# Performance work log

Measured on AMD Instinct MI355X. Metric: run time of the kernel, lower is better.

The kernel has to match this reference:

```python
import jax, jax.numpy as jnp
import numpy as np
import math

B, N, D = 2, 4096, 1024
NUM_LAYERS = 12
INIT_RANGE = 0.02


def setup_inputs() -> dict:
    key = jax.random.key(0)
    k1, k2 = jax.random.split(key)
    hidden_states = jax.random.normal(k1, (B, N, D), dtype=jnp.float32)
    std = INIT_RANGE / math.sqrt(2.0 * NUM_LAYERS * D)
    queries = jax.random.normal(k2, (D, D), dtype=jnp.float32) * std
    return {"hidden_states": hidden_states, "queries": queries}


def reference(hidden_states, queries):
    # Q = F.linear(X, W) = X @ W^T  -> [B, N, D]
    q = jnp.einsum('bnd,ed->bne', hidden_states, queries)
    # pre_attn = Q @ X^T  -> [B, N, N]
    pre_attn = jnp.einsum('bne,bme->bnm', q, hidden_states)
    # attention = pre_attn @ X  -> [B, N, D]
    attention = jnp.einsum('bnm,bmd->bnd', pre_attn, hidden_states)
    return attention
```

## Files before the change

### kernel.cpp

```cpp
#include <hip/hip_runtime.h>
#include <hip/hip_bf16.h>
#include <stdint.h>

using bf16 = __hip_bfloat16;
typedef __attribute__((ext_vector_type(8))) short short8;
typedef __attribute__((ext_vector_type(4))) float f32x4;

#define BM 128
#define BK 32

__device__ __forceinline__ void g2lds16(const void* g, void* l) {
    __builtin_amdgcn_global_load_lds(
        (const __attribute__((address_space(1))) void*)g,
        (__attribute__((address_space(3))) void*)l,
        16, 0, 0);
}

__device__ __forceinline__ short f2bs(float x) {
    union { bf16 h; short s; } u;
    u.h = __float2bfloat16(x);
    return u.s;
}

__device__ __forceinline__ int bswz(int row, int cg) { return cg ^ ((row >> 1) & 3); }
__device__ __forceinline__ int fswz(int row, int cg) { return cg ^ (row & 7); }

__global__ __launch_bounds__(256)
void transpose_cvt(const float* __restrict__ src, ushort* __restrict__ dstT,
                   ushort* __restrict__ dstN,
                   int R, int C, long sstride, long dstrideT, long dstrideN)
{
    __shared__ __align__(16) ushort t[64][72];
    const float* s = src + (size_t)blockIdx.z * sstride;
    ushort*      dT = dstT + (size_t)blockIdx.z * dstrideT;
    const int r0 = blockIdx.y * 64, c0 = blockIdx.x * 64;
    const int tid = threadIdx.x;
#pragma unroll
    for (int ii = 0; ii < 4; ++ii) {
        int idx = ii * 256 + tid;
        int r = idx >> 4, c4 = (idx & 15) * 4;
        float4 v = *(const float4*)&s[(size_t)(r0 + r) * C + c0 + c4];
        union { ushort u[4]; uint2 q; } o;
        o.u[0] = (ushort)f2bs(v.x); o.u[1] = (ushort)f2bs(v.y);
        o.u[2] = (ushort)f2bs(v.z); o.u[3] = (ushort)f2bs(v.w);
        *(uint2*)&t[r][c4] = o.q;
        if (dstN) {
            ushort* dN = dstN + (size_t)blockIdx.z * dstrideN;
            *(uint2*)&dN[(size_t)(r0 + r) * C + c0 + c4] = o.q;
        }
    }
    __syncthreads();
#pragma unroll
    for (int ii = 0; ii < 2; ++ii) {
        int idx = ii * 256 + tid;
        int c = idx >> 3, r8 = (idx & 7) * 8;
        union { ushort u[8]; uint4 v; } tmp;
#pragma unroll
        for (int j = 0; j < 8; ++j) tmp.u[j] = t[r8 + j][c];
        *(uint4*)&dT[(size_t)(c0 + c) * R + r0 + r8] = tmp.v;
    }
}

template <int MODE, int A_F32, int NFRAG>
__global__ __launch_bounds__(256)
void gemm_bt(const void* __restrict__ Av, const bf16* __restrict__ B,
             void* __restrict__ Cv, int M, int N, int K, int kChunks,
             long sA, long sB, long sC)
{
    constexpr int BN  = 32 * NFRAG;
    constexpr int BSH = BN / 64;
    constexpr int ANE = BM * BK * (A_F32 ? 2 : 1);
    __shared__ __align__(16) bf16 lA[2][ANE];
    __shared__ __align__(16) bf16 lB[2][BN * BK];

    const int z     = blockIdx.z;
    const int batch = z / kChunks;
    const int chunk = z - batch * kChunks;
    const int kLen  = K / kChunks;
    const int k0    = chunk * kLen;

    const int gx  = gridDim.x;
    int flat = blockIdx.y * gx + blockIdx.x;
    const int cpx = (gx * gridDim.y) >> 3;
    flat = (flat & 7) * cpx + (flat >> 3);
    const int m0 = (flat / gx) * BM;
    const int n0 = (flat - (flat / gx) * gx) * BN;

    const int tid  = threadIdx.x;
    const int lane = tid & 63;
    const int wave = tid >> 6;
    const int wr   = wave >> 1, wc = wave & 1;
    const int ml   = lane & 15;
    const int q    = lane >> 4;

    const bf16* Bb = B + (size_t)batch * sB;
    const bf16* bp[BSH];
#pragma unroll
    for (int s = 0; s < BSH; ++s) {
        int idx = s * 256 + tid;
        int row = idx >> 2, cg = idx & 3;
        bp[s] = Bb + (size_t)(n0 + row) * K + k0 + 8 * bswz(row, cg);
    }

    const float* a32[4];
    const bf16*  a16[2];
    if constexpr (A_F32) {
        const float* Ab = (const float*)Av + (size_t)batch * sA;
#pragma unroll
        for (int s = 0; s < 4; ++s) {
            int idx = s * 256 + tid;
            int row = idx >> 3, cg = idx & 7;
            a32[s] = Ab + (size_t)(m0 + row) * K + k0 + 4 * fswz(row, cg);
        }
    } else {
        const bf16* Ab = (const bf16*)Av + (size_t)batch * sA;
#pragma unroll
        for (int s = 0; s < 2; ++s) {
            int idx = s * 256 + tid;
            int row = idx >> 2, cg = idx & 3;
            a16[s] = Ab + (size_t)(m0 + row) * K + k0 + 8 * bswz(row, cg);
        }
    }

    f32x4 acc[4][NFRAG] = {};

    auto stage = [&](int buf) {
        if constexpr (A_F32) {
            float* lAf = (float*)lA[buf];
#pragma unroll
            for (int s = 0; s < 4; ++s) {
                g2lds16(a32[s], &lAf[(s * 256 + tid) * 4]);
                a32[s] += BK;
            }
        } else {
#pragma unroll
            for (int s = 0; s < 2; ++s) {
                g2lds16(a16[s], &lA[buf][(s * 256 + tid) * 8]);
                a16[s] += BK;
            }
        }
#pragma unroll
        for (int s = 0; s < BSH; ++s) {
            g2lds16(bp[s], &lB[buf][(s * 256 + tid) * 8]);
            bp[s] += BK;
        }
    };

    auto compute = [&](int buf) {
        const bf16* cA = lA[buf];
        const bf16* cB = lB[buf];
        short8 af[4], bfr[NFRAG];
#pragma unroll
        for (int i = 0; i < 4; ++i) {
            const int rA = wr * 64 + i * 16 + ml;
            if constexpr (A_F32) {
                const float* lAf = (const float*)cA;
                float4 x0 = *(const float4*)&lAf[rA * 32 + 4 * fswz(rA, 2 * q)];
                float4 x1 = *(const float4*)&lAf[rA * 32 + 4 * fswz(rA, 2 * q + 1)];
                af[i][0] = f2bs(x0.x); af[i][1] = f2bs(x0.y);
                af[i][2] = f2bs(x0.z); af[i][3] = f2bs(x0.w);
                af[i][4] = f2bs(x1.x); af[i][5] = f2bs(x1.y);
                af[i][6] = f2bs(x1.z); af[i][7] = f2bs(x1.w);
            } else {
                af[i] = *(const short8*)&cA[rA * 32 + 8 * bswz(rA, q)];
            }
        }
#pragma unroll
        for (int j = 0; j < NFRAG; ++j) {
            const int rB = wc * (16 * NFRAG) + j * 16 + ml;
            bfr[j] = *(const short8*)&cB[rB * 32 + 8 * bswz(rB, q)];
        }
#pragma unroll
        for (int mi = 0; mi < 4; ++mi)
#pragma unroll
            for (int nj = 0; nj < NFRAG; ++nj)
                acc[mi][nj] = __builtin_amdgcn_mfma_f32_16x16x32_bf16(
                    af[mi], bfr[nj], acc[mi][nj], 0, 0, 0);
    };

    const int nk = kLen / BK;
    stage(0);
    __syncthreads();
    int cur = 0;
    for (int kt = 0; kt < nk - 1; ++kt) {
        stage(cur ^ 1);
        compute(cur);
        __syncthreads();
        cur ^= 1;
    }
    compute(cur);

#pragma unroll
    for (int mi = 0; mi < 4; ++mi)
#pragma unroll
        for (int nj = 0; nj < NFRAG; ++nj)
#pragma unroll
            for (int r = 0; r < 4; ++r) {
                int row = m0 + wr * 64 + mi * 16 + q * 4 + r;
                int col = n0 + wc * (16 * NFRAG) + nj * 16 + ml;
                if constexpr (MODE == 1) {
                    float* Cf = (float*)Cv + (size_t)batch * sC;
                    atomicAdd(&Cf[(size_t)row * N + col], acc[mi][nj][r]);
                } else if constexpr (MODE == 0) {
                    ushort* Cb = (ushort*)Cv + (size_t)batch * sC;
                    Cb[(size_t)row * N + col] = (ushort)f2bs(acc[mi][nj][r]);
                } else {
                    float* Cf = (float*)Cv + (size_t)batch * sC;
                    Cf[(size_t)row * N + col] = acc[mi][nj][r];
                }
            }
}

extern "C" void kernel_launch(void* const* d_in, const int* in_sizes, int n_in,
                              void* d_out, int out_size, void* d_ws, size_t ws_size,
                              hipStream_t stream)
{
    const int B = 2, N = 4096, D = 1024;
    const float* X = (const float*)d_in[0];
    const float* W = (const float*)d_in[1];
    float* out = (float*)d_out;

    char* ob = (char*)d_out;
    char* ws = (char*)d_ws;
    ushort* Xt = (ushort*)ob;
    float*  Gf = (float*)(ob + (16ll << 20));
    ushort* Wt = (ushort*)(ob + (28ll << 20));

    const bool bigws = ws_size >= (20ull << 20);
    ushort* Xb = bigws ? (ushort*)ws : nullptr;
    ushort* Mt = (ushort*)(ws + (bigws ? (16ll << 20) : 0));

    transpose_cvt<<<dim3(D / 64, N / 64, B), 256, 0, stream>>>(
        X, Xt, Xb, N, D, (long)N * D, (long)D * N, (long)N * D);
    transpose_cvt<<<dim3(D / 64, D / 64, 1), 256, 0, stream>>>(
        W, Wt, nullptr, D, D, 0, 0, 0);
    (void)hipMemsetAsync(Gf, 0, (size_t)B * D * D * sizeof(float), stream);
    gemm_bt<1, 0, 4><<<dim3(D / 128, D / BM, B * 4), 256, 0, stream>>>(
        (const void*)Xt, (const bf16*)Xt, Gf, D, D, N, 4,
        (long)D * N, (long)D * N, (long)D * D);
    gemm_bt<0, 1, 2><<<dim3(D / 64, D / BM, B), 256, 0, stream>>>(
        (const void*)Gf, (const bf16*)Wt, Mt, D, D, D, 1,
        (long)D * D, 0, (long)D * D);
    if (bigws) {
        gemm_bt<2, 0, 4><<<dim3(D / 128, N / BM, B), 256, 0, stream>>>(
            (const void*)Xb, (const bf16*)Mt, out, N, D, D, 1,
            (long)N * D, (long)D * D, (long)N * D);
    } else {
        gemm_bt<2, 1, 4><<<dim3(D / 128, N / BM, B), 256, 0, stream>>>(
            (const void*)X, (const bf16*)Mt, out, N, D, D, 1,
            (long)N * D, (long)D * D, (long)N * D);
    }
}
```

Measured before the change: 203.1 us.

## Triple-buffer GEMM LDS stages with explicit vmcnt waits and MFMA priority

Replaces the double-buffered K loop with a three-stage LDS ring that prefetches two tiles ahead. Explicit s_waitcnt vmcnt counts and raw s_barrier calls replace __syncthreads. The next stage is issued right after the fragments are read into registers, before the MFMAs. MFMA blocks run at raised wave priority (s_setprio). The aim is to hide global-to-LDS latency and cut barrier stalls, at the cost of 50% more shared memory, which may lower occupancy, and fragile hand-counted wait values.

Result: faster. 182.6 us (-10.1%).

```diff
diff --git a/kernel.cpp b/kernel.cpp
--- a/kernel.cpp
+++ b/kernel.cpp
@@ -14,6 +14,15 @@
         (const __attribute__((address_space(1))) void*)g,
         (__attribute__((address_space(3))) void*)l,
         16, 0, 0);
+}
+
+template <int N>
+__device__ __forceinline__ void s_wait_vmcnt() {
+    asm volatile("s_waitcnt vmcnt(%0)" :: "n"(N) : "memory");
+}
+__device__ __forceinline__ void s_wait_lgkm0() {
+    asm volatile("s_waitcnt lgkmcnt(0)" ::: "memory");
+    __builtin_amdgcn_sched_barrier(0);
 }
 
 __device__ __forceinline__ short f2bs(float x) {
@@ -69,9 +78,11 @@
 {
     constexpr int BN  = 32 * NFRAG;
     constexpr int BSH = BN / 64;
+    constexpr int ASH = A_F32 ? 4 : 2;
+    constexpr int L   = ASH + BSH;
     constexpr int ANE = BM * BK * (A_F32 ? 2 : 1);
-    __shared__ __align__(16) bf16 lA[2][ANE];
-    __shared__ __align__(16) bf16 lB[2][BN * BK];
+    __shared__ __align__(16) bf16 lA[3][ANE];
+    __shared__ __align__(16) bf16 lB[3][BN * BK];
 
     const int z     = blockIdx.z;
     const int batch = z / kChunks;
@@ -146,7 +157,7 @@
         }
     };
 
-    auto compute = [&](int buf) {
+    auto step = [&](int buf, bool doStage) {
         const bf16* cA = lA[buf];
         const bf16* cB = lB[buf];
         short8 af[4], bfr[NFRAG];
@@ -170,25 +181,35 @@
             const int rB = wc * (16 * NFRAG) + j * 16 + ml;
             bfr[j] = *(const short8*)&cB[rB * 32 + 8 * bswz(rB, q)];
         }
+        s_wait_lgkm0();
+        __builtin_amdgcn_s_barrier();
+        if (doStage) stage(buf);
+        __builtin_amdgcn_s_setprio(1);
 #pragma unroll
         for (int mi = 0; mi < 4; ++mi)
 #pragma unroll
             for (int nj = 0; nj < NFRAG; ++nj)
                 acc[mi][nj] = __builtin_amdgcn_mfma_f32_16x16x32_bf16(
                     af[mi], bfr[nj], acc[mi][nj], 0, 0, 0);
+        __builtin_amdgcn_s_setprio(0);
     };
 
     const int nk = kLen / BK;
-    stage(0);
-    __syncthreads();
+    stage(0); stage(1); stage(2);
     int cur = 0;
-    for (int kt = 0; kt < nk - 1; ++kt) {
-        stage(cur ^ 1);
-        compute(cur);
-        __syncthreads();
-        cur ^= 1;
-    }
-    compute(cur);
+    for (int kt = 0; kt < nk - 2; ++kt) {
+        s_wait_vmcnt<2 * L>();
+        __builtin_amdgcn_s_barrier();
+        step(cur, kt < nk - 3);
+        cur = (cur == 2) ? 0 : cur + 1;
+    }
+    s_wait_vmcnt<L>();
+    __builtin_amdgcn_s_barrier();
+    step(cur, false);
+    cur = (cur == 2) ? 0 : cur + 1;
+    s_wait_vmcnt<0>();
+    __builtin_amdgcn_s_barrier();
+    step(cur, false);
 
 #pragma unroll
     for (int mi = 0; mi < 4; ++mi)
```

## Deepen GEMM LDS pipeline to four buffers with explicit vmcnt waits

Applied to the files above, without the earlier changes.

Replaces the double-buffered global-to-LDS staging with a four-stage ring of statically selected LDS buffers. Three tiles are prefetched ahead, and each step waits only on the oldest outstanding loads using s_waitcnt vmcnt instead of a full __syncthreads. This is meant to hide global load latency better and to cut barrier stalls. In exchange it doubles LDS use, which can lower occupancy, and it assumes nk is a multiple of 4 and at least 4.

Measured after the change: 174.7 us. 1.16x faster.

```diff
diff --git a/kernel.cpp b/kernel.cpp
--- a/kernel.cpp
+++ b/kernel.cpp
@@ -8,12 +8,19 @@
 
 #define BM 128
 #define BK 32
+
+template <int V> struct ic { static constexpr int v = V; };
 
 __device__ __forceinline__ void g2lds16(const void* g, void* l) {
     __builtin_amdgcn_global_load_lds(
         (const __attribute__((address_space(1))) void*)g,
         (__attribute__((address_space(3))) void*)l,
         16, 0, 0);
+}
+
+template <int N>
+__device__ __forceinline__ void s_wait_vmcnt() {
+    asm volatile("s_waitcnt vmcnt(%0)" :: "n"(N) : "memory");
 }
 
 __device__ __forceinline__ short f2bs(float x) {
@@ -69,9 +76,12 @@
 {
     constexpr int BN  = 32 * NFRAG;
     constexpr int BSH = BN / 64;
+    constexpr int ASH = A_F32 ? 4 : 2;
+    constexpr int L   = ASH + BSH;
     constexpr int ANE = BM * BK * (A_F32 ? 2 : 1);
-    __shared__ __align__(16) bf16 lA[2][ANE];
-    __shared__ __align__(16) bf16 lB[2][BN * BK];
+    constexpr int BNE = BN * BK;
+    __shared__ __align__(16) bf16 lA0[ANE], lA1[ANE], lA2[ANE], lA3[ANE];
+    __shared__ __align__(16) bf16 lB0[BNE], lB1[BNE], lB2[BNE], lB3[BNE];
 
     const int z     = blockIdx.z;
     const int batch = z / kChunks;
@@ -124,9 +134,26 @@
 
     f32x4 acc[4][NFRAG] = {};
 
-    auto stage = [&](int buf) {
+    auto pickA = [&](auto C) -> bf16* {
+        constexpr int b_ = decltype(C)::v;
+        if constexpr (b_ == 0) return lA0;
+        else if constexpr (b_ == 1) return lA1;
+        else if constexpr (b_ == 2) return lA2;
+        else return lA3;
+    };
+    auto pickB = [&](auto C) -> bf16* {
+        constexpr int b_ = decltype(C)::v;
+        if constexpr (b_ == 0) return lB0;
+        else if constexpr (b_ == 1) return lB1;
+        else if constexpr (b_ == 2) return lB2;
+        else return lB3;
+    };
+
+    auto stage = [&](auto C) {
+        bf16* A_ = pickA(C);
+        bf16* B_ = pickB(C);
         if constexpr (A_F32) {
-            float* lAf = (float*)lA[buf];
+            float* lAf = (float*)A_;
 #pragma unroll
             for (int s = 0; s < 4; ++s) {
                 g2lds16(a32[s], &lAf[(s * 256 + tid) * 4]);
@@ -135,21 +162,20 @@
         } else {
 #pragma unroll
             for (int s = 0; s < 2; ++s) {
-                g2lds16(a16[s], &lA[buf][(s * 256 + tid) * 8]);
+                g2lds16(a16[s], &A_[(s * 256 + tid) * 8]);
                 a16[s] += BK;
             }
         }
 #pragma unroll
         for (int s = 0; s < BSH; ++s) {
-            g2lds16(bp[s], &lB[buf][(s * 256 + tid) * 8]);
+            g2lds16(bp[s], &B_[(s * 256 + tid) * 8]);
             bp[s] += BK;
         }
     };
 
-    auto compute = [&](int buf) {
-        const bf16* cA = lA[buf];
-        const bf16* cB = lB[buf];
-        short8 af[4], bfr[NFRAG];
+    auto frags = [&](auto C, short8 (&af)[4], short8 (&bfr)[NFRAG]) {
+        const bf16* cA = pickA(C);
+        const bf16* cB = pickB(C);
 #pragma unroll
         for (int i = 0; i < 4; ++i) {
             const int rA = wr * 64 + i * 16 + ml;
@@ -170,6 +196,9 @@
             const int rB = wc * (16 * NFRAG) + j * 16 + ml;
             bfr[j] = *(const short8*)&cB[rB * 32 + 8 * bswz(rB, q)];
         }
+    };
+
+    auto mfma = [&](short8 (&af)[4], short8 (&bfr)[NFRAG]) {
 #pragma unroll
         for (int mi = 0; mi < 4; ++mi)
 #pragma unroll
@@ -178,17 +207,30 @@
                     af[mi], bfr[nj], acc[mi][nj], 0, 0, 0);
     };
 
+#define GB_STEP(BUF, DOSTAGE, VM)                                        \
+    do {                                                                 \
+        s_wait_vmcnt<(VM)>();                                            \
+        __builtin_amdgcn_s_barrier();                                    \
+        short8 af_[4], bf_[NFRAG];                                       \
+        frags(ic<BUF>{}, af_, bf_);                                      \
+        if (DOSTAGE) stage(ic<(BUF + 3) & 3>{});                         \
+        mfma(af_, bf_);                                                  \
+        asm volatile("s_waitcnt lgkmcnt(0)" ::: "memory");               \
+    } while (0)
+
     const int nk = kLen / BK;
-    stage(0);
-    __syncthreads();
-    int cur = 0;
-    for (int kt = 0; kt < nk - 1; ++kt) {
-        stage(cur ^ 1);
-        compute(cur);
-        __syncthreads();
-        cur ^= 1;
-    }
-    compute(cur);
+    stage(ic<0>{}); stage(ic<1>{}); stage(ic<2>{});
+    for (int t4 = 0; t4 < nk / 4 - 1; ++t4) {
+        GB_STEP(0, 1, 2 * L);
+        GB_STEP(1, 1, 2 * L);
+        GB_STEP(2, 1, 2 * L);
+        GB_STEP(3, 1, 2 * L);
+    }
+    GB_STEP(0, 1, 2 * L);
+    GB_STEP(1, 0, 2 * L);
+    GB_STEP(2, 0, L);
+    GB_STEP(3, 0, 0);
+#undef GB_STEP
 
 #pragma unroll
     for (int mi = 0; mi < 4; ++mi)
```

## Replace 4-wave GEMM blocks with single-wave 64x64 tiles using vmcnt-based pipelining

Applied to the files above, without the earlier changes.

All three GEMMs now use a single 64-thread wave per block, each computing a 64x64 output tile, instead of 256-thread blocks with 128x128 or 128x64 tiles. Block-wide barriers are removed. The double buffer is prefetched two stages ahead and synchronised with explicit s_waitcnt vmcnt/lgkmcnt instructions. The aim is to drop __syncthreads overhead and let many independent waves hide latency. The cost is no sharing of A/B tiles across waves, which raises global and L2 traffic per FLOP, and a four-times larger grid.

After: 206.8 us. No clear change (+1.8%).

```diff
diff --git a/kernel.cpp b/kernel.cpp
--- a/kernel.cpp
+++ b/kernel.cpp
@@ -6,7 +6,6 @@
 typedef __attribute__((ext_vector_type(8))) short short8;
 typedef __attribute__((ext_vector_type(4))) float f32x4;
 
-#define BM 128
 #define BK 32
 
 __device__ __forceinline__ void g2lds16(const void* g, void* l) {
@@ -14,6 +13,11 @@
         (const __attribute__((address_space(1))) void*)g,
         (__attribute__((address_space(3))) void*)l,
         16, 0, 0);
+}
+
+template <int N>
+__device__ __forceinline__ void s_wait_vmcnt() {
+    asm volatile("s_waitcnt vmcnt(%0)" :: "n"(N) : "memory");
 }
 
 __device__ __forceinline__ short f2bs(float x) {
@@ -61,17 +65,18 @@
     }
 }
 
-template <int MODE, int A_F32, int NFRAG>
-__global__ __launch_bounds__(256)
-void gemm_bt(const void* __restrict__ Av, const bf16* __restrict__ B,
+template <int MODE, int A_F32>
+__global__ __launch_bounds__(64)
+void gemm_w1(const void* __restrict__ Av, const bf16* __restrict__ B,
              void* __restrict__ Cv, int M, int N, int K, int kChunks,
              long sA, long sB, long sC)
 {
-    constexpr int BN  = 32 * NFRAG;
-    constexpr int BSH = BN / 64;
-    constexpr int ANE = BM * BK * (A_F32 ? 2 : 1);
+    constexpr int BSH = 4;
+    constexpr int ASH = A_F32 ? 8 : 4;
+    constexpr int L   = ASH + BSH;
+    constexpr int ANE = 64 * BK * (A_F32 ? 2 : 1);
     __shared__ __align__(16) bf16 lA[2][ANE];
-    __shared__ __align__(16) bf16 lB[2][BN * BK];
+    __shared__ __align__(16) bf16 lB[2][64 * BK];
 
     const int z     = blockIdx.z;
     const int batch = z / kChunks;
@@ -83,13 +88,10 @@
     int flat = blockIdx.y * gx + blockIdx.x;
     const int cpx = (gx * gridDim.y) >> 3;
     flat = (flat & 7) * cpx + (flat >> 3);
-    const int m0 = (flat / gx) * BM;
-    const int n0 = (flat - (flat / gx) * gx) * BN;
-
-    const int tid  = threadIdx.x;
-    const int lane = tid & 63;
-    const int wave = tid >> 6;
-    const int wr   = wave >> 1, wc = wave & 1;
+    const int m0 = (flat / gx) * 64;
+    const int n0 = (flat - (flat / gx) * gx) * 64;
+
+    const int lane = threadIdx.x;
     const int ml   = lane & 15;
     const int q    = lane >> 4;
 
@@ -97,62 +99,61 @@
     const bf16* bp[BSH];
 #pragma unroll
     for (int s = 0; s < BSH; ++s) {
-        int idx = s * 256 + tid;
+        int idx = s * 64 + lane;
         int row = idx >> 2, cg = idx & 3;
         bp[s] = Bb + (size_t)(n0 + row) * K + k0 + 8 * bswz(row, cg);
     }
 
-    const float* a32[4];
-    const bf16*  a16[2];
+    const float* a32[8];
+    const bf16*  a16[4];
     if constexpr (A_F32) {
         const float* Ab = (const float*)Av + (size_t)batch * sA;
 #pragma unroll
-        for (int s = 0; s < 4; ++s) {
-            int idx = s * 256 + tid;
+        for (int s = 0; s < 8; ++s) {
+            int idx = s * 64 + lane;
             int row = idx >> 3, cg = idx & 7;
             a32[s] = Ab + (size_t)(m0 + row) * K + k0 + 4 * fswz(row, cg);
         }
     } else {
         const bf16* Ab = (const bf16*)Av + (size_t)batch * sA;
 #pragma unroll
-        for (int s = 0; s < 2; ++s) {
-            int idx = s * 256 + tid;
+        for (int s = 0; s < 4; ++s) {
+            int idx = s * 64 + lane;
             int row = idx >> 2, cg = idx & 3;
             a16[s] = Ab + (size_t)(m0 + row) * K + k0 + 8 * bswz(row, cg);
         }
     }
 
-    f32x4 acc[4][NFRAG] = {};
+    f32x4 acc[4][4] = {};
 
     auto stage = [&](int buf) {
         if constexpr (A_F32) {
             float* lAf = (float*)lA[buf];
 #pragma unroll
+            for (int s = 0; s < 8; ++s) {
+                g2lds16(a32[s], &lAf[(s * 64 + lane) * 4]);
+                a32[s] += BK;
+            }
+        } else {
+#pragma unroll
             for (int s = 0; s < 4; ++s) {
-                g2lds16(a32[s], &lAf[(s * 256 + tid) * 4]);
-                a32[s] += BK;
-            }
-        } else {
-#pragma unroll
-            for (int s = 0; s < 2; ++s) {
-                g2lds16(a16[s], &lA[buf][(s * 256 + tid) * 8]);
+                g2lds16(a16[s], &lA[buf][(s * 64 + lane) * 8]);
                 a16[s] += BK;
             }
         }
 #pragma unroll
         for (int s = 0; s < BSH; ++s) {
-            g2lds16(bp[s], &lB[buf][(s * 256 + tid) * 8]);
+            g2lds16(bp[s], &lB[buf][(s * 64 + lane) * 8]);
             bp[s] += BK;
         }
     };
 
-    auto compute = [&](int buf) {
+    auto frags = [&](int buf, short8 (&af)[4], short8 (&bfr)[4]) {
         const bf16* cA = lA[buf];
         const bf16* cB = lB[buf];
-        short8 af[4], bfr[NFRAG];
 #pragma unroll
         for (int i = 0; i < 4; ++i) {
-            const int rA = wr * 64 + i * 16 + ml;
+            const int rA = i * 16 + ml;
             if constexpr (A_F32) {
                 const float* lAf = (const float*)cA;
                 float4 x0 = *(const float4*)&lAf[rA * 32 + 4 * fswz(rA, 2 * q)];
@@ -166,38 +167,43 @@
             }
         }
 #pragma unroll
-        for (int j = 0; j < NFRAG; ++j) {
-            const int rB = wc * (16 * NFRAG) + j * 16 + ml;
+        for (int j = 0; j < 4; ++j) {
+            const int rB = j * 16 + ml;
             bfr[j] = *(const short8*)&cB[rB * 32 + 8 * bswz(rB, q)];
         }
+    };
+
+    auto mfma = [&](short8 (&af)[4], short8 (&bfr)[4]) {
 #pragma unroll
         for (int mi = 0; mi < 4; ++mi)
 #pragma unroll
-            for (int nj = 0; nj < NFRAG; ++nj)
+            for (int nj = 0; nj < 4; ++nj)
                 acc[mi][nj] = __builtin_amdgcn_mfma_f32_16x16x32_bf16(
                     af[mi], bfr[nj], acc[mi][nj], 0, 0, 0);
     };
 
     const int nk = kLen / BK;
-    stage(0);
-    __syncthreads();
-    int cur = 0;
-    for (int kt = 0; kt < nk - 1; ++kt) {
-        stage(cur ^ 1);
-        compute(cur);
-        __syncthreads();
-        cur ^= 1;
-    }
-    compute(cur);
+    stage(0); stage(1);
+    for (int t = 0; t < nk; ++t) {
+        if (t < nk - 1) s_wait_vmcnt<L>();
+        else            s_wait_vmcnt<0>();
+        short8 af_[4], bf_[4];
+        frags(t & 1, af_, bf_);
+        mfma(af_, bf_);
+        if (t < nk - 2) {
+            asm volatile("s_waitcnt lgkmcnt(0)" ::: "memory");
+            stage(t & 1);
+        }
+    }
 
 #pragma unroll
     for (int mi = 0; mi < 4; ++mi)
 #pragma unroll
-        for (int nj = 0; nj < NFRAG; ++nj)
+        for (int nj = 0; nj < 4; ++nj)
 #pragma unroll
             for (int r = 0; r < 4; ++r) {
-                int row = m0 + wr * 64 + mi * 16 + q * 4 + r;
-                int col = n0 + wc * (16 * NFRAG) + nj * 16 + ml;
+                int row = m0 + mi * 16 + q * 4 + r;
+                int col = n0 + nj * 16 + ml;
                 if constexpr (MODE == 1) {
                     float* Cf = (float*)Cv + (size_t)batch * sC;
                     atomicAdd(&Cf[(size_t)row * N + col], acc[mi][nj][r]);
@@ -235,18 +241,18 @@
     transpose_cvt<<<dim3(D / 64, D / 64, 1), 256, 0, stream>>>(
         W, Wt, nullptr, D, D, 0, 0, 0);
     (void)hipMemsetAsync(Gf, 0, (size_t)B * D * D * sizeof(float), stream);
-    gemm_bt<1, 0, 4><<<dim3(D / 128, D / BM, B * 4), 256, 0, stream>>>(
+    gemm_w1<1, 0><<<dim3(D / 64, D / 64, B * 4), 64, 0, stream>>>(
         (const void*)Xt, (const bf16*)Xt, Gf, D, D, N, 4,
         (long)D * N, (long)D * N, (long)D * D);
-    gemm_bt<0, 1, 2><<<dim3(D / 64, D / BM, B), 256, 0, stream>>>(
+    gemm_w1<0, 1><<<dim3(D / 64, D / 64, B), 64, 0, stream>>>(
         (const void*)Gf, (const bf16*)Wt, Mt, D, D, D, 1,
         (long)D * D, 0, (long)D * D);
     if (bigws) {
-        gemm_bt<2, 0, 4><<<dim3(D / 128, N / BM, B), 256, 0, stream>>>(
+        gemm_w1<2, 0><<<dim3(D / 64, N / 64, B), 64, 0, stream>>>(
             (const void*)Xb, (const bf16*)Mt, out, N, D, D, 1,
             (long)N * D, (long)D * D, (long)N * D);
     } else {
-        gemm_bt<2, 1, 4><<<dim3(D / 128, N / BM, B), 256, 0, stream>>>(
+        gemm_w1<2, 1><<<dim3(D / 64, N / 64, B), 64, 0, stream>>>(
             (const void*)X, (const bf16*)Mt, out, N, D, D, 1,
             (long)N * D, (long)D * D, (long)N * D);
     }
```
